# Kernel tuning notes

Measured on AMD Instinct MI355X. Metric: run time of the kernel, lower is better.

The kernel has to match this reference:

```python
import jax, jax.numpy as jnp
import numpy as np

B = 1024      # batch
E = 1024      # encoding_dim
OUT = 34      # 17 joints x 2 coords


def setup_inputs() -> dict:
    key = jax.random.key(0)
    ks = jax.random.split(key, 8)
    s = 0.02  # weight init scale
    return {
        "h": jax.random.normal(ks[0], (B, E), dtype=jnp.float32),
        "c": jax.random.normal(ks[1], (B, E), dtype=jnp.float32),
        "W_ih": jax.random.normal(ks[2], (4 * E, E), dtype=jnp.float32) * s,
        "W_hh": jax.random.normal(ks[3], (4 * E, E), dtype=jnp.float32) * s,
        "b_ih": jax.random.normal(ks[4], (4 * E,), dtype=jnp.float32) * s,
        "b_hh": jax.random.normal(ks[5], (4 * E,), dtype=jnp.float32) * s,
        "W_out": jax.random.normal(ks[6], (OUT, E), dtype=jnp.float32) * s,
        "b_out": jax.random.normal(ks[7], (OUT,), dtype=jnp.float32) * s,
        "future_preds": 10,
    }


def reference(h, c, W_ih, W_hh, b_ih, b_hh, W_out, b_out, future_preds):
    E_ = h.shape[1]
    start = jnp.zeros_like(h)  # zeros=True start token

    def step(carry, _):
        h_t, c_t, x = carry
        # LSTMCell: gates in PyTorch order i, f, g, o
        gates = x @ W_ih.T + b_ih + h_t @ W_hh.T + b_hh  # [B, 4E]
        i = jax.nn.sigmoid(gates[:, 0 * E_:1 * E_])
        f = jax.nn.sigmoid(gates[:, 1 * E_:2 * E_])
        g = jnp.tanh(gates[:, 2 * E_:3 * E_])
        o = jax.nn.sigmoid(gates[:, 3 * E_:4 * E_])
        c_new = f * c_t + i * g
        h_new = o * jnp.tanh(c_new)
        return (h_new, c_new, h_new), h_new

    _, hs = jax.lax.scan(step, (h, c, start), None, length=future_preds)
    # hs: [T, B, E] -> [B, T, E]
    preds = jnp.transpose(hs, (1, 0, 2))
    return preds @ W_out.T + b_out  # [B, T, 34]
```

## Files before the change

### kernel.cpp

```cpp
#include <hip/hip_runtime.h>
#include <cstdint>
#include <cstddef>

#define E_DIM   1024
#define B_DIM   1024
#define HPITCH  1040
#define T_STEPS 10
#define OUT_DIM 34
#define OUT_PAD 48
#define HSTR    24
#define WSLICE  65536
#define HT_ROWS 256
#define DYN_LDS (WSLICE * 2 + HT_ROWS * HSTR * 2)
#define HSLOT  ((size_t)B_DIM * HPITCH)

typedef __attribute__((ext_vector_type(4))) float  f32x4;
typedef __attribute__((ext_vector_type(8))) __bf16 bf16x8;

__device__ __forceinline__ unsigned short f2bf(float f) {
    unsigned int u = __float_as_uint(f);
    u = (u + 0x7FFFu + ((u >> 16) & 1u)) >> 16;
    return (unsigned short)u;
}
__device__ __forceinline__ float sigmoid_(float x) { return 1.0f / (1.0f + __expf(-x)); }
__device__ __forceinline__ float tanh_(float x)    { return 2.0f / (1.0f + __expf(-2.0f * x)) - 1.0f; }

__global__ void prep_all(const float* __restrict__ W_ih, const float* __restrict__ W_hh,
                         const float* __restrict__ h0, const float* __restrict__ c0,
                         const float* __restrict__ W_out,
                         const float* __restrict__ b_ih, const float* __restrict__ b_hh,
                         unsigned short* __restrict__ WsumF, unsigned short* __restrict__ WhhF,
                         unsigned short* __restrict__ hbuf, unsigned short* __restrict__ Woutp,
                         float* __restrict__ bperm, float* __restrict__ C) {
    const int blk = blockIdx.x;
    const int t = threadIdx.x;
    if (blk < 512) {
        const int bn = blk >> 3, qtr = (blk >> 1) & 3, half = blk & 1;
        const int nt = t >> 6, lane = t & 63;
        const int j = lane & 15, q = lane >> 4;
        const int srow = nt * E_DIM + bn * 16 + j;
        const float* wi = W_ih + (size_t)srow * E_DIM;
        const float* wh = W_hh + (size_t)srow * E_DIM;
        const size_t dstb = (size_t)bn * 65536 + (size_t)qtr * 16384 + nt * 512 + lane * 8;
#pragma unroll
        for (int ks8i = 0; ks8i < 4; ++ks8i) {
            const int ks8 = half * 4 + ks8i;
            const int k = qtr * 256 + ks8 * 32 + q * 8;
            float4 i0 = *(const float4*)(wi + k);
            float4 i1 = *(const float4*)(wi + k + 4);
            float4 h0v = *(const float4*)(wh + k);
            float4 h1v = *(const float4*)(wh + k + 4);
            unsigned short* ds = WsumF + dstb + ks8 * 2048;
            unsigned short* dh = WhhF  + dstb + ks8 * 2048;
            ds[0] = f2bf(i0.x + h0v.x); ds[1] = f2bf(i0.y + h0v.y);
            ds[2] = f2bf(i0.z + h0v.z); ds[3] = f2bf(i0.w + h0v.w);
            ds[4] = f2bf(i1.x + h1v.x); ds[5] = f2bf(i1.y + h1v.y);
            ds[6] = f2bf(i1.z + h1v.z); ds[7] = f2bf(i1.w + h1v.w);
            dh[0] = f2bf(h0v.x); dh[1] = f2bf(h0v.y); dh[2] = f2bf(h0v.z); dh[3] = f2bf(h0v.w);
            dh[4] = f2bf(h1v.x); dh[5] = f2bf(h1v.y); dh[6] = f2bf(h1v.z); dh[7] = f2bf(h1v.w);
        }
        return;
    }
    const int b = blk - 512;
    if (b < 1024) {
        const size_t src = ((size_t)b * 256 + t) * 4;
        float4 hv = *(const float4*)(h0 + src);
        const size_t i = (size_t)b * HPITCH + t * 4;
        hbuf[i + 0] = f2bf(hv.x);
        hbuf[i + 1] = f2bf(hv.y);
        hbuf[i + 2] = f2bf(hv.z);
        hbuf[i + 3] = f2bf(hv.w);
    } else if (b < 1072) {
        const int o = b - 1024;
        const int k = t * 4;
        float4 w = make_float4(0.f, 0.f, 0.f, 0.f);
        if (o < OUT_DIM) w = *(const float4*)(W_out + (size_t)o * E_DIM + k);
        const size_t dst = (size_t)o * E_DIM + k;
        Woutp[dst + 0] = f2bf(w.x);
        Woutp[dst + 1] = f2bf(w.y);
        Woutp[dst + 2] = f2bf(w.z);
        Woutp[dst + 3] = f2bf(w.w);
    } else if (b < 1088) {
        const int n = (b - 1072) * 256 + t;
        const int g = (n >> 4) & 3;
        const int e = ((n >> 6) << 4) | (n & 15);
        const int srow = g * E_DIM + e;
        bperm[n] = b_ih[srow] + b_hh[srow];
    } else {
        const int m = b - 1088;
        const int e0 = t * 4;
        float4 v = *(const float4*)(c0 + (size_t)m * E_DIM + e0);
        const int bm = m >> 7, wave = (m >> 5) & 3, mt = (m >> 4) & 1, q = (m >> 2) & 3, r = m & 3;
        const float vv[4] = {v.x, v.y, v.z, v.w};
#pragma unroll
        for (int ii = 0; ii < 4; ++ii) {
            const int e = e0 + ii;
            const int bn = e >> 4, jj = e & 15;
            const int lane = q * 16 + jj;
            C[(((size_t)(bn * 8 + bm) * 4 + wave) * 64 + lane) * 8 + mt * 4 + r] = vv[ii];
        }
    }
}

__global__ __launch_bounds__(512, 2) void lstm_step(
    const unsigned short* __restrict__ WF,
    const float* __restrict__ bp,
    const unsigned short* __restrict__ Hin,
    float* __restrict__ C,
    unsigned short* __restrict__ Hout)
{
    extern __shared__ __align__(16) unsigned short smem[];
    unsigned short* Wlds = smem;
    unsigned short* Ht   = smem + WSLICE;

    const int tid  = threadIdx.x;
    const int w    = tid >> 6;
    const int lane = tid & 63;
    const int bn = blockIdx.x;
    const int g  = blockIdx.y;
    const int j  = lane & 15;
    const int q  = lane >> 4;

    f32x4 acc[2][4];
#pragma unroll
    for (int a = 0; a < 2; ++a)
#pragma unroll
        for (int b = 0; b < 4; ++b) acc[a][b] = (f32x4){0.f, 0.f, 0.f, 0.f};

    const int nb = bn * 64 + j;
    const float bi = bp[nb +  0];
    const float bf = bp[nb + 16];
    const float bg = bp[nb + 32];
    const float bo = bp[nb + 48];
    const int obm = g * 2 + (w >> 2), owv = w & 3;
    const size_t cbase = (((size_t)(bn * 8 + obm) * 4 + owv) * 64 + lane) * 8;
    float4 cold0 = *(const float4*)(C + cbase);
    float4 cold1 = *(const float4*)(C + cbase + 4);

    const unsigned short* arow0 = Hin + (size_t)(g * 256 + w * 32 + j) * HPITCH + q * 8;
    const unsigned short* arow1 = arow0 + (size_t)16 * HPITCH;
    const unsigned short* wsrc  = WF + (size_t)bn * WSLICE;

    {
        uint4 wreg[8];
#pragma unroll
        for (int r2 = 0; r2 < 2; ++r2) {
#pragma unroll
            for (int i = 0; i < 8; ++i)
                wreg[i] = *(const uint4*)(wsrc + ((r2 * 8 + i) * 512 + tid) * 8);
#pragma unroll
            for (int i = 0; i < 8; ++i)
                *(uint4*)(Wlds + ((r2 * 8 + i) * 512 + tid) * 8) = wreg[i];
        }
    }

    uint4 ra[8][2];
#pragma unroll
    for (int p = 0; p < 8; ++p) {
        ra[p][0] = *(const uint4*)(arow0 + p * 32);
        ra[p][1] = *(const uint4*)(arow1 + p * 32);
    }
    __syncthreads();

    for (int qtr = 0; qtr < 4; ++qtr) {
        const unsigned short* wb = Wlds + qtr * 16384 + lane * 8;
#pragma unroll
        for (int ks8 = 0; ks8 < 8; ++ks8) {
            const int ks = qtr * 8 + ks8;
            bf16x8 av0 = __builtin_bit_cast(bf16x8, ra[ks8][0]);
            bf16x8 av1 = __builtin_bit_cast(bf16x8, ra[ks8][1]);
            bf16x8 bv[4];
#pragma unroll
            for (int nt = 0; nt < 4; ++nt)
                bv[nt] = *(const bf16x8*)(wb + (ks8 * 4 + nt) * 512);
#pragma unroll
            for (int nt = 0; nt < 4; ++nt) {
                acc[0][nt] = __builtin_amdgcn_mfma_f32_16x16x32_bf16(av0, bv[nt], acc[0][nt], 0, 0, 0);
                acc[1][nt] = __builtin_amdgcn_mfma_f32_16x16x32_bf16(av1, bv[nt], acc[1][nt], 0, 0, 0);
            }
            if (ks < 24) {
                ra[ks8][0] = *(const uint4*)(arow0 + (ks + 8) * 32);
                ra[ks8][1] = *(const uint4*)(arow1 + (ks + 8) * 32);
            }
        }
    }

    float4 cnew[2];
    const float coldv[2][4] = {{cold0.x, cold0.y, cold0.z, cold0.w},
                               {cold1.x, cold1.y, cold1.z, cold1.w}};
#pragma unroll
    for (int mt = 0; mt < 2; ++mt) {
#pragma unroll
        for (int r = 0; r < 4; ++r) {
            const float iv = sigmoid_(acc[mt][0][r] + bi);
            const float fv = sigmoid_(acc[mt][1][r] + bf);
            const float gv = tanh_(acc[mt][2][r] + bg);
            const float ov = sigmoid_(acc[mt][3][r] + bo);
            const float cn = fv * coldv[mt][r] + iv * gv;
            cnew[mt][r] = cn;
            const int rowl = w * 32 + mt * 16 + q * 4 + r;
            Ht[rowl * HSTR + j] = f2bf(ov * tanh_(cn));
        }
    }
    *(float4*)(C + cbase)     = cnew[0];
    *(float4*)(C + cbase + 4) = cnew[1];
    __syncthreads();

    {
        const int row = tid >> 1, part = tid & 1;
        uint4 v = *(const uint4*)(Ht + row * HSTR + part * 8);
        *(uint4*)(Hout + (size_t)(g * 256 + row) * HPITCH + bn * 16 + part * 8) = v;
    }
}

__global__ __launch_bounds__(256) void proj_kernel(
    const unsigned short* __restrict__ Hs,
    const unsigned short* __restrict__ Wo,
    const float* __restrict__ b_out,
    float* __restrict__ Out)
{
    __shared__ float red[4][32][OUT_PAD];

    const int tid = threadIdx.x, wave = tid >> 6, lane = tid & 63;
    const int j = lane & 15, q = lane >> 4;
    const int t  = blockIdx.y;
    const int bb = blockIdx.x;
    const unsigned short* Hbase = Hs + (size_t)t * HSLOT + (size_t)bb * 32 * HPITCH;
    const int k0 = wave * 256;

    f32x4 acc[2][3];
#pragma unroll
    for (int a = 0; a < 2; ++a)
#pragma unroll
        for (int b = 0; b < 3; ++b) acc[a][b] = (f32x4){0.f, 0.f, 0.f, 0.f};

#pragma unroll
    for (int kk = 0; kk < 256; kk += 32) {
        const int kc = k0 + kk + q * 8;
        bf16x8 av[2], bv[3];
#pragma unroll
        for (int mt = 0; mt < 2; ++mt)
            av[mt] = *(const bf16x8*)(Hbase + (size_t)(mt * 16 + j) * HPITCH + kc);
#pragma unroll
        for (int nt = 0; nt < 3; ++nt)
            bv[nt] = *(const bf16x8*)(Wo + (size_t)(nt * 16 + j) * E_DIM + kc);
#pragma unroll
        for (int mt = 0; mt < 2; ++mt)
#pragma unroll
            for (int nt = 0; nt < 3; ++nt)
                acc[mt][nt] = __builtin_amdgcn_mfma_f32_16x16x32_bf16(av[mt], bv[nt], acc[mt][nt], 0, 0, 0);
    }

#pragma unroll
    for (int mt = 0; mt < 2; ++mt)
#pragma unroll
        for (int nt = 0; nt < 3; ++nt)
#pragma unroll
            for (int r = 0; r < 4; ++r)
                red[wave][mt * 16 + q * 4 + r][nt * 16 + j] = acc[mt][nt][r];
    __syncthreads();

#pragma unroll
    for (int ii = 0; ii < 6; ++ii) {
        const int idx = tid * 6 + ii;
        const int row = idx / OUT_PAD, o = idx % OUT_PAD;
        if (o < OUT_DIM) {
            const float s = red[0][row][o] + red[1][row][o] + red[2][row][o] + red[3][row][o];
            Out[((size_t)(bb * 32 + row) * T_STEPS + t) * OUT_DIM + o] = s + b_out[o];
        }
    }
}

extern "C" void kernel_launch(void* const* d_in, const int* in_sizes, int n_in,
                              void* d_out, int out_size, void* d_ws, size_t ws_size,
                              hipStream_t stream) {
    (void)in_sizes; (void)n_in; (void)out_size; (void)ws_size;
    const float* h     = (const float*)d_in[0];
    const float* c     = (const float*)d_in[1];
    const float* W_ih  = (const float*)d_in[2];
    const float* W_hh  = (const float*)d_in[3];
    const float* b_ih  = (const float*)d_in[4];
    const float* b_hh  = (const float*)d_in[5];
    const float* W_out = (const float*)d_in[6];
    const float* b_out = (const float*)d_in[7];
    float* out = (float*)d_out;

    char* ws = (char*)d_ws;
    unsigned short* WsumF = (unsigned short*)(ws + 0);
    unsigned short* WhhF  = (unsigned short*)(ws + 8388608);
    float*          bperm = (float*)(ws + 16777216);
    unsigned short* Woutp = (unsigned short*)(ws + 16842752);
    float*          cbuf  = (float*)(ws + 16941056);
    unsigned short* hs    = (unsigned short*)(ws + 21135360);

    hipFuncSetAttribute((const void*)lstm_step,
                        hipFuncAttributeMaxDynamicSharedMemorySize, DYN_LDS);

    prep_all<<<2624, 256, 0, stream>>>(W_ih, W_hh, h, c, W_out, b_ih, b_hh,
                                       WsumF, WhhF, hs, Woutp, bperm, cbuf);

    lstm_step<<<dim3(64, 4), 512, DYN_LDS, stream>>>(WhhF, bperm, hs, cbuf, hs + HSLOT);
    for (int t = 1; t < T_STEPS; ++t)
        lstm_step<<<dim3(64, 4), 512, DYN_LDS, stream>>>(WsumF, bperm,
                                                         hs + (size_t)t * HSLOT,
                                                         cbuf,
                                                         hs + (size_t)(t + 1) * HSLOT);

    proj_kernel<<<dim3(32, T_STEPS), 256, 0, stream>>>(hs + HSLOT, Woutp, b_out, out);
}
```

Baseline: 273.5 us.

## Split K across wave pairs to raise weight-fragment reuse in LSTM step

```diff
diff --git a/kernel.cpp b/kernel.cpp
--- a/kernel.cpp
+++ b/kernel.cpp
@@ -112,18 +112,21 @@
     extern __shared__ __align__(16) unsigned short smem[];
     unsigned short* Wlds = smem;
     unsigned short* Ht   = smem + WSLICE;
+    float* X = (float*)smem;
 
     const int tid  = threadIdx.x;
     const int w    = tid >> 6;
     const int lane = tid & 63;
+    const int wk   = w & 1;
+    const int wm   = w >> 1;
     const int bn = blockIdx.x;
     const int g  = blockIdx.y;
     const int j  = lane & 15;
     const int q  = lane >> 4;
 
-    f32x4 acc[2][4];
-#pragma unroll
-    for (int a = 0; a < 2; ++a)
+    f32x4 acc[4][4];
+#pragma unroll
+    for (int a = 0; a < 4; ++a)
 #pragma unroll
         for (int b = 0; b < 4; ++b) acc[a][b] = (f32x4){0.f, 0.f, 0.f, 0.f};
 
@@ -137,9 +140,13 @@
     float4 cold0 = *(const float4*)(C + cbase);
     float4 cold1 = *(const float4*)(C + cbase + 4);
 
-    const unsigned short* arow0 = Hin + (size_t)(g * 256 + w * 32 + j) * HPITCH + q * 8;
-    const unsigned short* arow1 = arow0 + (size_t)16 * HPITCH;
-    const unsigned short* wsrc  = WF + (size_t)bn * WSLICE;
+    const unsigned short* arow[4];
+    arow[0] = Hin + (size_t)(g * 256 + wm * 64 + j) * HPITCH + wk * 512 + q * 8;
+#pragma unroll
+    for (int mt = 1; mt < 4; ++mt)
+        arow[mt] = arow[mt - 1] + (size_t)16 * HPITCH;
+
+    const unsigned short* wsrc = WF + (size_t)bn * WSLICE;
 
     {
         uint4 wreg[8];
@@ -154,34 +161,56 @@
         }
     }
 
-    uint4 ra[8][2];
-#pragma unroll
-    for (int p = 0; p < 8; ++p) {
-        ra[p][0] = *(const uint4*)(arow0 + p * 32);
-        ra[p][1] = *(const uint4*)(arow1 + p * 32);
-    }
-    __syncthreads();
-
-    for (int qtr = 0; qtr < 4; ++qtr) {
-        const unsigned short* wb = Wlds + qtr * 16384 + lane * 8;
-#pragma unroll
-        for (int ks8 = 0; ks8 < 8; ++ks8) {
-            const int ks = qtr * 8 + ks8;
-            bf16x8 av0 = __builtin_bit_cast(bf16x8, ra[ks8][0]);
-            bf16x8 av1 = __builtin_bit_cast(bf16x8, ra[ks8][1]);
-            bf16x8 bv[4];
+    uint4 ra[4][4];
+#pragma unroll
+    for (int p = 0; p < 4; ++p)
+#pragma unroll
+        for (int mt = 0; mt < 4; ++mt)
+            ra[mt][p] = *(const uint4*)(arow[mt] + p * 32);
+    __syncthreads();
+
+    const unsigned short* wbase = Wlds + wk * 32768 + lane * 8;
+#pragma unroll
+    for (int ks = 0; ks < 16; ++ks) {
+        const unsigned short* wb = wbase + (ks >> 3) * 16384 + (ks & 7) * 2048;
+        bf16x8 bv[4];
+#pragma unroll
+        for (int nt = 0; nt < 4; ++nt)
+            bv[nt] = *(const bf16x8*)(wb + nt * 512);
+#pragma unroll
+        for (int mt = 0; mt < 4; ++mt) {
+            bf16x8 av = __builtin_bit_cast(bf16x8, ra[mt][ks & 3]);
 #pragma unroll
             for (int nt = 0; nt < 4; ++nt)
-                bv[nt] = *(const bf16x8*)(wb + (ks8 * 4 + nt) * 512);
-#pragma unroll
-            for (int nt = 0; nt < 4; ++nt) {
-                acc[0][nt] = __builtin_amdgcn_mfma_f32_16x16x32_bf16(av0, bv[nt], acc[0][nt], 0, 0, 0);
-                acc[1][nt] = __builtin_amdgcn_mfma_f32_16x16x32_bf16(av1, bv[nt], acc[1][nt], 0, 0, 0);
-            }
-            if (ks < 24) {
-                ra[ks8][0] = *(const uint4*)(arow0 + (ks + 8) * 32);
-                ra[ks8][1] = *(const uint4*)(arow1 + (ks + 8) * 32);
-            }
+                acc[mt][nt] = __builtin_amdgcn_mfma_f32_16x16x32_bf16(av, bv[nt], acc[mt][nt], 0, 0, 0);
+        }
+        if (ks < 12) {
+#pragma unroll
+            for (int mt = 0; mt < 4; ++mt)
+                ra[mt][ks & 3] = *(const uint4*)(arow[mt] + (ks + 4) * 32);
+        }
+    }
+    __syncthreads();
+
+    {
+        float* dst = X + (wm * 2 + wk) * 2048;
+#pragma unroll
+        for (int mtl = 0; mtl < 2; ++mtl) {
+            const int mt = (1 - wk) * 2 + mtl;
+#pragma unroll
+            for (int nt = 0; nt < 4; ++nt)
+                *(f32x4*)(dst + ((mtl * 4 + nt) * 64 + lane) * 4) = acc[mt][nt];
+        }
+    }
+    __syncthreads();
+    {
+        const float* src = X + (wm * 2 + (1 - wk)) * 2048;
+#pragma unroll
+        for (int mtl = 0; mtl < 2; ++mtl) {
+            const int mt = wk * 2 + mtl;
+#pragma unroll
+            for (int nt = 0; nt < 4; ++nt)
+                acc[mt][nt] += *(const f32x4*)(src + ((mtl * 4 + nt) * 64 + lane) * 4);
         }
     }
 
@@ -189,16 +218,17 @@
     const float coldv[2][4] = {{cold0.x, cold0.y, cold0.z, cold0.w},
                                {cold1.x, cold1.y, cold1.z, cold1.w}};
 #pragma unroll
-    for (int mt = 0; mt < 2; ++mt) {
+    for (int mtl = 0; mtl < 2; ++mtl) {
+        const int mt = wk * 2 + mtl;
 #pragma unroll
         for (int r = 0; r < 4; ++r) {
             const float iv = sigmoid_(acc[mt][0][r] + bi);
             const float fv = sigmoid_(acc[mt][1][r] + bf);
             const float gv = tanh_(acc[mt][2][r] + bg);
             const float ov = sigmoid_(acc[mt][3][r] + bo);
-            const float cn = fv * coldv[mt][r] + iv * gv;
-            cnew[mt][r] = cn;
-            const int rowl = w * 32 + mt * 16 + q * 4 + r;
+            const float cn = fv * coldv[mtl][r] + iv * gv;
+            cnew[mtl][r] = cn;
+            const int rowl = w * 32 + mtl * 16 + q * 4 + r;
             Ht[rowl * HSTR + j] = f2bf(ov * tanh_(cn));
         }
     }
```

Result: slower. 800.7 us (+192.7%).
